# Kernel tuning notes

Hardware: AMD Instinct MI355X
Metric: run time of the kernel (lower is better)

Reference implementation:

```python
import jax, jax.numpy as jnp
import numpy as np

B, T, D, H = 64, 512, 512, 1024


def setup_inputs() -> dict:
    key = jax.random.key(0)
    k1, k2, k3 = jax.random.split(key, 3)
    x = jax.random.normal(k1, (B, T, D), dtype=jnp.float32)
    W = jax.random.normal(k2, (D, 4 * H), dtype=jnp.float32) * 0.02  # input kernel
    U = jax.random.normal(k3, (H, 4 * H), dtype=jnp.float32) * 0.02  # recurrent kernel
    b = jnp.zeros((4 * H,), dtype=jnp.float32)
    return {"x": x, "W": W, "U": U, "b": b}


def reference(x, W, U, b):
    # Keras LSTM, gate order [i, f, c(g), o], sigmoid recurrent activation, tanh activation.
    # return_sequences=False, return_state=True -> pred == h_T; output = concat([h_T, h_T, c_T]).
    batch = x.shape[0]
    hidden = U.shape[0]

    def step(carry, xt):
        h, c = carry
        z = xt @ W + h @ U + b  # [B, 4H]
        i, f, g, o = jnp.split(z, 4, axis=-1)
        i = jax.nn.sigmoid(i)
        f = jax.nn.sigmoid(f)
        o = jax.nn.sigmoid(o)
        c_new = f * c + i * jnp.tanh(g)
        h_new = o * jnp.tanh(c_new)
        return (h_new, c_new), None

    h0 = jnp.zeros((batch, hidden), dtype=x.dtype)
    c0 = jnp.zeros((batch, hidden), dtype=x.dtype)
    xs = jnp.swapaxes(x, 0, 1)  # [T, B, D]
    (hT, cT), _ = jax.lax.scan(step, (h0, c0), xs)
    return jnp.concatenate([hT, hT, cT], axis=-1)  # [B, 3H]
```

## Files before the change

### kernel.cpp

```cpp
#include <hip/hip_runtime.h>
#include <stdint.h>

typedef unsigned short u16;

#define T_STEPS 512
#define BATCH   64
#define DIN     512
#define HID     1024
#define G4      4096
#define THREADS 512
#define GRPS    2
#define NBG     64
#define UPB     16

#define U_LD    1032
#define W_LD    520

#define SM_BYTES 66048
#define HS_OFF   35328

#define XB_BYTES ((size_t)T_STEPS * BATCH * DIN * 2)
#define HB_OFF   XB_BYTES
#define HB_GRP   (2u * 32 * HID * 2)
#define FLG_OFF  (HB_OFF + (size_t)GRPS * HB_GRP)
#define FLG_GRP  1024
#define WS_NEED  (FLG_OFF + (size_t)GRPS * FLG_GRP)

typedef float f32x16 __attribute__((ext_vector_type(16)));
typedef short bf16x8 __attribute__((ext_vector_type(8)));
typedef unsigned uint32x4 __attribute__((ext_vector_type(4)));

__device__ __forceinline__ u16 f2bf(float f) {
  unsigned u = __float_as_uint(f);
  u += 0x7fffu + ((u >> 16) & 1u);
  return (u16)(u >> 16);
}
__device__ __forceinline__ float sigm(float x) {
  return __builtin_amdgcn_rcpf(1.f + __expf(-x));
}
__device__ __forceinline__ float fast_tanh(float x) {
  return 1.f - 2.f * __builtin_amdgcn_rcpf(__expf(2.f * x) + 1.f);
}

__device__ __forceinline__ uint32x4 load16_sc(uint64_t addr) {
  uint32x4 d;
  asm volatile("global_load_dwordx4 %0, %1, off sc0 sc1" : "=v"(d) : "v"(addr));
  return d;
}
__device__ __forceinline__ unsigned load4_sc(uint64_t addr) {
  unsigned d;
  asm volatile("global_load_dword %0, %1, off sc0 sc1" : "=v"(d) : "v"(addr));
  return d;
}
__device__ __forceinline__ void store16_sc(uint64_t addr, uint32x4 v) {
  asm volatile("global_store_dwordx4 %0, %1, off sc0 sc1" :: "v"(addr), "v"(v) : "memory");
}
__device__ __forceinline__ void store4_sc(uint64_t addr, unsigned v) {
  asm volatile("global_store_dword %0, %1, off sc0 sc1" :: "v"(addr), "v"(v) : "memory");
}
#define WAITV(n) asm volatile("s_waitcnt vmcnt(" #n ")" ::: "memory")

__global__ void cvt_x(const float* __restrict__ x, u16* __restrict__ xb) {
  int i = blockIdx.x * 256 + threadIdx.x;
  int dblk = i & 63;
  int rest = i >> 6;
  int b = rest & 63;
  int t = rest >> 6;
  const float4* s = reinterpret_cast<const float4*>(x + ((size_t)(b * T_STEPS + t)) * DIN + dblk * 8);
  float4 f0 = s[0], f1 = s[1];
  uint4 o;
  o.x = (unsigned)f2bf(f0.x) | ((unsigned)f2bf(f0.y) << 16);
  o.y = (unsigned)f2bf(f0.z) | ((unsigned)f2bf(f0.w) << 16);
  o.z = (unsigned)f2bf(f1.x) | ((unsigned)f2bf(f1.y) << 16);
  o.w = (unsigned)f2bf(f1.z) | ((unsigned)f2bf(f1.w) << 16);
  *reinterpret_cast<uint4*>(xb + ((size_t)(t * BATCH + b)) * DIN + dblk * 8) = o;
}

__launch_bounds__(THREADS)
__global__ void lstm_kernel(const float* __restrict__ W, const float* __restrict__ U,
                            const float* __restrict__ bias, char* __restrict__ ws,
                            float* __restrict__ out) {
  __shared__ __align__(16) char sm[SM_BYTES];
  u16* stage  = (u16*)sm;
  float* zp   = (float*)sm;
  u16* hstage = (u16*)(sm + HS_OFF);

  const int tid = threadIdx.x;
  const int bid = blockIdx.x;
  const int nb  = bid & 63;
  const int grp = bid >> 6;

  const int l    = tid & 63;
  const int wv   = tid >> 6;
  const int n_t  = wv & 1;
  const int ks   = wv >> 1;
  const int cl   = l & 31;
  const int q    = l >> 5;

  bf16x8 ubf[16], wbf[8];
#pragma unroll
  for (int ph = 0; ph < 2; ++ph) {
    for (int idx = tid; idx < 32 * HID; idx += THREADS) {
      int cc = idx & 31, k = idx >> 5;
      int c = ph * 32 + cc;
      int gcol = ((c & 3) << 10) + nb * UPB + (c >> 2);
      stage[cc * U_LD + k] = f2bf(U[(size_t)k * G4 + gcol]);
    }
    __syncthreads();
    if (n_t == ph) {
      const u16* ub = stage + cl * U_LD + ks * 256 + q * 8;
#pragma unroll
      for (int s = 0; s < 16; ++s) ubf[s] = *(const bf16x8*)(ub + s * 16);
    }
    __syncthreads();
  }
#pragma unroll
  for (int ph = 0; ph < 2; ++ph) {
    for (int idx = tid; idx < 32 * DIN; idx += THREADS) {
      int cc = idx & 31, k = idx >> 5;
      int c = ph * 32 + cc;
      int gcol = ((c & 3) << 10) + nb * UPB + (c >> 2);
      stage[cc * W_LD + k] = f2bf(W[(size_t)k * G4 + gcol]);
    }
    __syncthreads();
    if (n_t == ph) {
      const u16* wb = stage + cl * W_LD + ks * 128 + q * 8;
#pragma unroll
      for (int s = 0; s < 8; ++s) wbf[s] = *(const bf16x8*)(wb + s * 16);
    }
    __syncthreads();
  }

  const int pb = tid & 31;
  const int pu = tid >> 5;
  const int j  = nb * UPB + pu;
  float c_reg = 0.f;
  const float bi  = bias[j];
  const float bf_ = bias[1024 + j];
  const float bg  = bias[2048 + j];
  const float bo  = bias[3072 + j];

  const u16* xb = (const u16*)ws;
  const uint64_t hgrp = (uint64_t)ws + HB_OFF + (uint64_t)grp * HB_GRP;
  const uint64_t fgrp = (uint64_t)ws + FLG_OFF + (uint64_t)grp * FLG_GRP;
  const uint64_t faddr = fgrp + (uint64_t)(ks * 16 + (l & 15)) * 16;
  const uint64_t hlane = (uint64_t)(ks * 32 + q) * 512 + (uint64_t)cl * 16;

#define HMFMA(S) acc = __builtin_amdgcn_mfma_f32_32x32x16_bf16( \
    __builtin_bit_cast(bf16x8, abuf[S]), ubf[S], acc, 0, 0, 0)

  for (int t = 0; t < T_STEPS; ++t) {
    f32x16 acc = {0.f,0.f,0.f,0.f,0.f,0.f,0.f,0.f,0.f,0.f,0.f,0.f,0.f,0.f,0.f,0.f};

    const u16* xa = xb + ((size_t)t * BATCH + grp * 32 + cl) * DIN + ks * 128 + q * 8;
#pragma unroll
    for (int s = 0; s < 8; ++s) {
      bf16x8 xv = *(const bf16x8*)(xa + s * 16);
      acc = __builtin_amdgcn_mfma_f32_32x32x16_bf16(xv, wbf[s], acc, 0, 0, 0);
    }

    while (true) {
      unsigned f = load4_sc(faddr);
      WAITV(0);
      if (__all(f >= (unsigned)t)) break;
      __builtin_amdgcn_s_sleep(1);
    }

    const uint64_t hb = hgrp + (uint64_t)(t & 1) * 65536 + hlane;
    uint32x4 abuf[16];
#pragma unroll
    for (int s = 0; s < 16; ++s) abuf[s] = load16_sc(hb + (uint64_t)s * 1024);
    WAITV(12); __builtin_amdgcn_sched_barrier(0);
    HMFMA(0); HMFMA(1); HMFMA(2); HMFMA(3);
    WAITV(8); __builtin_amdgcn_sched_barrier(0);
    HMFMA(4); HMFMA(5); HMFMA(6); HMFMA(7);
    WAITV(4); __builtin_amdgcn_sched_barrier(0);
    HMFMA(8); HMFMA(9); HMFMA(10); HMFMA(11);
    WAITV(0); __builtin_amdgcn_sched_barrier(0);
    HMFMA(12); HMFMA(13); HMFMA(14); HMFMA(15);

#pragma unroll
    for (int r = 0; r < 16; ++r) {
      int rl = (r & 3) + 8 * (r >> 2) + 4 * q;
      zp[ks * 2208 + rl * 69 + n_t * 32 + cl] = acc[r];
    }
    __syncthreads();

    float zi = bi, zf = bf_, zg = bg, zo = bo;
#pragma unroll
    for (int k2 = 0; k2 < 4; ++k2) {
      float4 zv = *(const float4*)(zp + k2 * 2208 + pb * 69 + pu * 4);
      zi += zv.x; zf += zv.y; zg += zv.z; zo += zv.w;
    }
    float ig = sigm(zi), fg = sigm(zf), og = sigm(zo);
    float gg = fast_tanh(zg);
    c_reg = fg * c_reg + ig * gg;
    float h = og * fast_tanh(c_reg);
    hstage[(pu >> 3) * 256 + pb * 8 + (pu & 7)] = f2bf(h);
    if (t == T_STEPS - 1) {
      float* orow = out + (size_t)(grp * 32 + pb) * 3072 + j;
      orow[0]    = h;
      orow[1024] = h;
      orow[2048] = c_reg;
    }
    __syncthreads();

    if (wv == 0) {
      uint32x4 hv = *(const uint32x4*)(hstage + l * 8);
      uint64_t dst = hgrp + (uint64_t)((t + 1) & 1) * 65536 +
                     (uint64_t)nb * 1024 + (uint64_t)l * 16;
      store16_sc(dst, hv);
      WAITV(0);
      if (l == 0) store4_sc(fgrp + (uint64_t)nb * 16, (unsigned)(t + 1));
    }
  }
#undef HMFMA
}

extern "C" void kernel_launch(void* const* d_in, const int* in_sizes, int n_in,
                              void* d_out, int out_size, void* d_ws, size_t ws_size,
                              hipStream_t stream) {
  const float* x = (const float*)d_in[0];
  const float* W = (const float*)d_in[1];
  const float* U = (const float*)d_in[2];
  const float* b = (const float*)d_in[3];
  float* out = (float*)d_out;

  if (ws_size < WS_NEED) return;

  u16* xb = (u16*)d_ws;
  hipMemsetAsync((char*)d_ws + HB_OFF, 0, WS_NEED - HB_OFF, stream);
  cvt_x<<<(T_STEPS * BATCH * DIN / 8 + 255) / 256, 256, 0, stream>>>(x, xb);
  lstm_kernel<<<GRPS * NBG, THREADS, 0, stream>>>(W, U, b, (char*)d_ws, out);
}
```

Before: 2.778 ms.

## Interleave two batch halves per block and defer h publication to overlap sync

Drops the two independent 64-block batch groups in favour of 64 blocks, each handling both 32-row batch halves in alternating phases. While one half computes, the other half's h-state publication and flag wait can proceed, and each block's store and flag write are deferred into the next phase. W and U are pre-transposed to bf16 in gate-interleaved order by a separate prep kernel, so blocks load weights directly into registers instead of staging them through shared memory. Each wave now covers a smaller k-slice for two column tiles, with an 8-way shared-memory reduction. The risks are fewer CUs in use, and halving the grid could remove parallelism.

After: 3.341 ms. 20.3% more time.

```diff
diff --git a/kernel.cpp b/kernel.cpp
--- a/kernel.cpp
+++ b/kernel.cpp
@@ -9,22 +9,19 @@
 #define HID     1024
 #define G4      4096
 #define THREADS 512
-#define GRPS    2
-#define NBG     64
+#define NBLK    64
 #define UPB     16
 
-#define U_LD    1032
-#define W_LD    520
-
-#define SM_BYTES 66048
-#define HS_OFF   35328
-
-#define XB_BYTES ((size_t)T_STEPS * BATCH * DIN * 2)
-#define HB_OFF   XB_BYTES
-#define HB_GRP   (2u * 32 * HID * 2)
-#define FLG_OFF  (HB_OFF + (size_t)GRPS * HB_GRP)
-#define FLG_GRP  1024
-#define WS_NEED  (FLG_OFF + (size_t)GRPS * FLG_GRP)
+#define XB_BYTES  ((size_t)T_STEPS * BATCH * DIN * 2)
+#define WPR_OFF   XB_BYTES
+#define WPR_BYTES ((size_t)4096 * 512 * 2)
+#define UPR_OFF   (WPR_OFF + WPR_BYTES)
+#define UPR_BYTES ((size_t)4096 * 1024 * 2)
+#define H_OFF     (UPR_OFF + UPR_BYTES)
+#define H_BYTES   (4u * 65536)
+#define F_OFF     (H_OFF + H_BYTES)
+#define F_BYTES   2048
+#define WS_NEED   (F_OFF + F_BYTES)
 
 typedef float f32x16 __attribute__((ext_vector_type(16)));
 typedef short bf16x8 __attribute__((ext_vector_type(8)));
@@ -76,145 +73,164 @@
   *reinterpret_cast<uint4*>(xb + ((size_t)(t * BATCH + b)) * DIN + dblk * 8) = o;
 }
 
-__launch_bounds__(THREADS)
-__global__ void lstm_kernel(const float* __restrict__ W, const float* __restrict__ U,
-                            const float* __restrict__ bias, char* __restrict__ ws,
-                            float* __restrict__ out) {
-  __shared__ __align__(16) char sm[SM_BYTES];
-  u16* stage  = (u16*)sm;
-  float* zp   = (float*)sm;
-  u16* hstage = (u16*)(sm + HS_OFF);
-
+__global__ void prep_t(const float* __restrict__ src, u16* __restrict__ dst, int K) {
+  __shared__ u16 tl[64][72];
+  const int kb = blockIdx.x >> 6, cb = blockIdx.x & 63;
   const int tid = threadIdx.x;
-  const int bid = blockIdx.x;
-  const int nb  = bid & 63;
-  const int grp = bid >> 6;
-
-  const int l    = tid & 63;
-  const int wv   = tid >> 6;
-  const int n_t  = wv & 1;
-  const int ks   = wv >> 1;
-  const int cl   = l & 31;
-  const int q    = l >> 5;
-
-  bf16x8 ubf[16], wbf[8];
-#pragma unroll
-  for (int ph = 0; ph < 2; ++ph) {
-    for (int idx = tid; idx < 32 * HID; idx += THREADS) {
-      int cc = idx & 31, k = idx >> 5;
-      int c = ph * 32 + cc;
-      int gcol = ((c & 3) << 10) + nb * UPB + (c >> 2);
-      stage[cc * U_LD + k] = f2bf(U[(size_t)k * G4 + gcol]);
-    }
-    __syncthreads();
-    if (n_t == ph) {
-      const u16* ub = stage + cl * U_LD + ks * 256 + q * 8;
-#pragma unroll
-      for (int s = 0; s < 16; ++s) ubf[s] = *(const bf16x8*)(ub + s * 16);
-    }
-    __syncthreads();
-  }
-#pragma unroll
-  for (int ph = 0; ph < 2; ++ph) {
-    for (int idx = tid; idx < 32 * DIN; idx += THREADS) {
-      int cc = idx & 31, k = idx >> 5;
-      int c = ph * 32 + cc;
-      int gcol = ((c & 3) << 10) + nb * UPB + (c >> 2);
-      stage[cc * W_LD + k] = f2bf(W[(size_t)k * G4 + gcol]);
-    }
-    __syncthreads();
-    if (n_t == ph) {
-      const u16* wb = stage + cl * W_LD + ks * 128 + q * 8;
-#pragma unroll
-      for (int s = 0; s < 8; ++s) wbf[s] = *(const bf16x8*)(wb + s * 16);
-    }
-    __syncthreads();
+  {
+    const int kl = tid >> 2, j0 = (tid & 3) * 16;
+    const float* s = src + (size_t)(kb * 64 + kl) * 4096 + cb * 64 + j0;
+#pragma unroll
+    for (int c = 0; c < 16; c += 4) {
+      float4 v = *(const float4*)(s + c);
+      tl[j0 + c + 0][kl] = f2bf(v.x);
+      tl[j0 + c + 1][kl] = f2bf(v.y);
+      tl[j0 + c + 2][kl] = f2bf(v.z);
+      tl[j0 + c + 3][kl] = f2bf(v.w);
+    }
+  }
+  __syncthreads();
+  {
+    const int j = tid >> 2, kp = (tid & 3) * 16;
+    const int gcol = cb * 64 + j;
+    const int p = (gcol & 1023) * 4 + (gcol >> 10);
+    const uint4* s = (const uint4*)&tl[j][kp];
+    uint4* d = (uint4*)(dst + (size_t)p * K + kb * 64 + kp);
+    d[0] = s[0];
+    d[1] = s[1];
+  }
+}
+
+__launch_bounds__(THREADS, 2)
+__global__ void lstm_kernel(const u16* __restrict__ upr, const u16* __restrict__ wpr,
+                            const float* __restrict__ bias, const u16* __restrict__ xb,
+                            char* __restrict__ ws, float* __restrict__ out) {
+  __shared__ float zp[8][32][68];
+  __shared__ u16 hst[2][512];
+
+  const int tid = threadIdx.x;
+  const int nb  = blockIdx.x;
+  const int l   = tid & 63;
+  const int wv  = tid >> 6;
+  const int cl  = l & 31;
+  const int q   = l >> 5;
+
+  bf16x8 ubf[2][8], wbf[2][4];
+#pragma unroll
+  for (int tile = 0; tile < 2; ++tile) {
+    const u16* ub = upr + (size_t)(nb * 64 + tile * 32 + cl) * 1024 + wv * 128 + q * 8;
+#pragma unroll
+    for (int s = 0; s < 8; ++s) ubf[tile][s] = *(const bf16x8*)(ub + s * 16);
+    const u16* wb = wpr + (size_t)(nb * 64 + tile * 32 + cl) * 512 + wv * 64 + q * 8;
+#pragma unroll
+    for (int s = 0; s < 4; ++s) wbf[tile][s] = *(const bf16x8*)(wb + s * 16);
   }
 
   const int pb = tid & 31;
   const int pu = tid >> 5;
   const int j  = nb * UPB + pu;
-  float c_reg = 0.f;
   const float bi  = bias[j];
   const float bf_ = bias[1024 + j];
   const float bg  = bias[2048 + j];
   const float bo  = bias[3072 + j];
-
-  const u16* xb = (const u16*)ws;
-  const uint64_t hgrp = (uint64_t)ws + HB_OFF + (uint64_t)grp * HB_GRP;
-  const uint64_t fgrp = (uint64_t)ws + FLG_OFF + (uint64_t)grp * FLG_GRP;
-  const uint64_t faddr = fgrp + (uint64_t)(ks * 16 + (l & 15)) * 16;
-  const uint64_t hlane = (uint64_t)(ks * 32 + q) * 512 + (uint64_t)cl * 16;
-
-#define HMFMA(S) acc = __builtin_amdgcn_mfma_f32_32x32x16_bf16( \
-    __builtin_bit_cast(bf16x8, abuf[S]), ubf[S], acc, 0, 0, 0)
-
-  for (int t = 0; t < T_STEPS; ++t) {
-    f32x16 acc = {0.f,0.f,0.f,0.f,0.f,0.f,0.f,0.f,0.f,0.f,0.f,0.f,0.f,0.f,0.f,0.f};
-
-    const u16* xa = xb + ((size_t)t * BATCH + grp * 32 + cl) * DIN + ks * 128 + q * 8;
-#pragma unroll
-    for (int s = 0; s < 8; ++s) {
-      bf16x8 xv = *(const bf16x8*)(xa + s * 16);
-      acc = __builtin_amdgcn_mfma_f32_32x32x16_bf16(xv, wbf[s], acc, 0, 0, 0);
-    }
-
-    while (true) {
-      unsigned f = load4_sc(faddr);
-      WAITV(0);
-      if (__all(f >= (unsigned)t)) break;
-      __builtin_amdgcn_s_sleep(1);
-    }
-
-    const uint64_t hb = hgrp + (uint64_t)(t & 1) * 65536 + hlane;
-    uint32x4 abuf[16];
-#pragma unroll
-    for (int s = 0; s < 16; ++s) abuf[s] = load16_sc(hb + (uint64_t)s * 1024);
-    WAITV(12); __builtin_amdgcn_sched_barrier(0);
-    HMFMA(0); HMFMA(1); HMFMA(2); HMFMA(3);
-    WAITV(8); __builtin_amdgcn_sched_barrier(0);
-    HMFMA(4); HMFMA(5); HMFMA(6); HMFMA(7);
+  float c0 = 0.f, c1 = 0.f;
+
+  const uint64_t hbase = (uint64_t)ws + H_OFF;
+  const uint64_t fbase = (uint64_t)ws + F_OFF;
+  const uint64_t puboff = (uint64_t)(nb >> 1) * 2048 + (uint64_t)(l >> 1) * 64 +
+                          (uint64_t)(nb & 1) * 32 + (uint64_t)(l & 1) * 16;
+
+  uint32x4 pubv = {0, 0, 0, 0};
+  uint64_t pubdst = 0, pubfl = 0;
+  unsigned pubtag = 0;
+
+  for (int phase = 0; phase < 2 * T_STEPS; ++phase) {
+    const int ch = phase & 1;
+    const int t  = phase >> 1;
+    const uint64_t hb = hbase + (uint64_t)ch * 131072 + (uint64_t)(t & 1) * 65536;
+
+    if (wv == 7 && phase) store16_sc(pubdst, pubv);
+
+    bf16x8 xf[4];
+    {
+      const u16* xr = xb + ((size_t)(t * 64 + ch * 32 + cl)) * 512 + wv * 64 + q * 8;
+#pragma unroll
+      for (int s = 0; s < 4; ++s) xf[s] = *(const bf16x8*)(xr + s * 16);
+    }
+
+    {
+      const uint64_t fa = fbase + (uint64_t)ch * 1024 + (uint64_t)(wv * 8 + (l & 7)) * 16;
+      while (true) {
+        unsigned f = load4_sc(fa);
+        WAITV(0);
+        if (__all(f >= (unsigned)t)) break;
+        __builtin_amdgcn_s_sleep(1);
+      }
+    }
+    if (wv == 7 && phase) store4_sc(pubfl, pubtag);
+
+    uint32x4 hbuf[8];
+#pragma unroll
+    for (int s = 0; s < 8; ++s)
+      hbuf[s] = load16_sc(hb + (uint64_t)((wv * 4 + (s >> 1)) * 2048) +
+                          (uint64_t)cl * 64 + (uint64_t)((s & 1) * 32 + q * 16));
+
+    f32x16 acc0 = {0.f,0.f,0.f,0.f,0.f,0.f,0.f,0.f,0.f,0.f,0.f,0.f,0.f,0.f,0.f,0.f};
+    f32x16 acc1 = {0.f,0.f,0.f,0.f,0.f,0.f,0.f,0.f,0.f,0.f,0.f,0.f,0.f,0.f,0.f,0.f};
+#pragma unroll
+    for (int s = 0; s < 4; ++s) {
+      acc0 = __builtin_amdgcn_mfma_f32_32x32x16_bf16(xf[s], wbf[0][s], acc0, 0, 0, 0);
+      acc1 = __builtin_amdgcn_mfma_f32_32x32x16_bf16(xf[s], wbf[1][s], acc1, 0, 0, 0);
+    }
     WAITV(4); __builtin_amdgcn_sched_barrier(0);
-    HMFMA(8); HMFMA(9); HMFMA(10); HMFMA(11);
+#pragma unroll
+    for (int s = 0; s < 4; ++s) {
+      bf16x8 a = __builtin_bit_cast(bf16x8, hbuf[s]);
+      acc0 = __builtin_amdgcn_mfma_f32_32x32x16_bf16(a, ubf[0][s], acc0, 0, 0, 0);
+      acc1 = __builtin_amdgcn_mfma_f32_32x32x16_bf16(a, ubf[1][s], acc1, 0, 0, 0);
+    }
     WAITV(0); __builtin_amdgcn_sched_barrier(0);
-    HMFMA(12); HMFMA(13); HMFMA(14); HMFMA(15);
+#pragma unroll
+    for (int s = 4; s < 8; ++s) {
+      bf16x8 a = __builtin_bit_cast(bf16x8, hbuf[s]);
+      acc0 = __builtin_amdgcn_mfma_f32_32x32x16_bf16(a, ubf[0][s], acc0, 0, 0, 0);
+      acc1 = __builtin_amdgcn_mfma_f32_32x32x16_bf16(a, ubf[1][s], acc1, 0, 0, 0);
+    }
 
 #pragma unroll
     for (int r = 0; r < 16; ++r) {
       int rl = (r & 3) + 8 * (r >> 2) + 4 * q;
-      zp[ks * 2208 + rl * 69 + n_t * 32 + cl] = acc[r];
+      zp[wv][rl][cl]      = acc0[r];
+      zp[wv][rl][32 + cl] = acc1[r];
     }
     __syncthreads();
 
     float zi = bi, zf = bf_, zg = bg, zo = bo;
 #pragma unroll
-    for (int k2 = 0; k2 < 4; ++k2) {
-      float4 zv = *(const float4*)(zp + k2 * 2208 + pb * 69 + pu * 4);
-      zi += zv.x; zf += zv.y; zg += zv.z; zo += zv.w;
+    for (int k2 = 0; k2 < 8; ++k2) {
+      float4 v = *(const float4*)&zp[k2][pb][pu * 4];
+      zi += v.x; zf += v.y; zg += v.z; zo += v.w;
     }
     float ig = sigm(zi), fg = sigm(zf), og = sigm(zo);
     float gg = fast_tanh(zg);
-    c_reg = fg * c_reg + ig * gg;
-    float h = og * fast_tanh(c_reg);
-    hstage[(pu >> 3) * 256 + pb * 8 + (pu & 7)] = f2bf(h);
+    float cr = ch ? c1 : c0;
+    cr = fg * cr + ig * gg;
+    float h = og * fast_tanh(cr);
+    if (ch) c1 = cr; else c0 = cr;
+    hst[ch][pb * 16 + pu] = f2bf(h);
     if (t == T_STEPS - 1) {
-      float* orow = out + (size_t)(grp * 32 + pb) * 3072 + j;
+      float* orow = out + (size_t)(ch * 32 + pb) * 3072 + j;
       orow[0]    = h;
       orow[1024] = h;
-      orow[2048] = c_reg;
+      orow[2048] = cr;
     }
     __syncthreads();
 
-    if (wv == 0) {
-      uint32x4 hv = *(const uint32x4*)(hstage + l * 8);
-      uint64_t dst = hgrp + (uint64_t)((t + 1) & 1) * 65536 +
-                     (uint64_t)nb * 1024 + (uint64_t)l * 16;
-      store16_sc(dst, hv);
-      WAITV(0);
-      if (l == 0) store4_sc(fgrp + (uint64_t)nb * 16, (unsigned)(t + 1));
-    }
-  }
-#undef HMFMA
+    pubv   = *(const uint32x4*)&hst[ch][l * 8];
+    pubdst = hbase + (uint64_t)ch * 131072 + (uint64_t)((t + 1) & 1) * 65536 + puboff;
+    pubfl  = fbase + (uint64_t)ch * 1024 + (uint64_t)nb * 16;
+    pubtag = (unsigned)(t + 1);
+  }
 }
 
 extern "C" void kernel_launch(void* const* d_in, const int* in_sizes, int n_in,
@@ -228,8 +244,13 @@
 
   if (ws_size < WS_NEED) return;
 
-  u16* xb = (u16*)d_ws;
-  hipMemsetAsync((char*)d_ws + HB_OFF, 0, WS_NEED - HB_OFF, stream);
+  u16* xb  = (u16*)d_ws;
+  u16* wpr = (u16*)((char*)d_ws + WPR_OFF);
+  u16* upr = (u16*)((char*)d_ws + UPR_OFF);
+
+  hipMemsetAsync((char*)d_ws + H_OFF, 0, H_BYTES + F_BYTES, stream);
   cvt_x<<<(T_STEPS * BATCH * DIN / 8 + 255) / 256, 256, 0, stream>>>(x, xb);
-  lstm_kernel<<<GRPS * NBG, THREADS, 0, stream>>>(W, U, b, (char*)d_ws, out);
-}
+  prep_t<<<(512 / 64) * 64, 256, 0, stream>>>(W, wpr, 512);
+  prep_t<<<(1024 / 64) * 64, 256, 0, stream>>>(U, upr, 1024);
+  lstm_kernel<<<NBLK, THREADS, 0, stream>>>(upr, wpr, b, xb, (char*)d_ws, out);
+}
```
